# Performance work log

Hardware: AMD Instinct MI355X
Metric: run time of the kernel (lower is better)

## Reference

```python
import jax, jax.numpy as jnp
import numpy as np

C, G, S, L, B = 16, 8192, 8, 3, 32


def setup_inputs() -> dict:
    key = jax.random.key(0)
    kx, kI = jax.random.split(key)
    # x: valuation vector over G ground atoms per batch element, in [0,1)
    x = jax.random.uniform(kx, (B, G), dtype=jnp.float32)
    # I: precomputed index tensor [C, G, S, L], indices into the G axis of x
    I = jax.random.randint(kI, (C, G, S, L), 0, G, dtype=jnp.int64)
    return {"x": x, "I": I}


def reference(x, I):
    # Equivalent of: for each clause i, gather(V_tild, 1, I_i) -> prod over L -> sum over S
    # torch gather semantics: out[b, g, s, l] = x[b, I[i, g, s, l]]
    # Vectorized over all clauses at once; no repeat/broadcast materialization beyond the gather.
    gathered = x[:, I]                        # [B, C, G, S, L]
    body = jnp.prod(gathered, axis=-1)        # conjunction over L body literals -> [B, C, G, S]
    clause_val = jnp.sum(body, axis=-1)       # sum over S substitutions -> [B, C, G]
    # torch.stack over clauses puts C first: [C, B, G]
    return jnp.transpose(clause_val, (1, 0, 2))
```

## Files before the change

kernel.cpp:

```cpp
#include <hip/hip_runtime.h>
#include <hip/hip_fp16.h>
#include <stdint.h>

#define Cc 16
#define Gg 8192
#define Ss 8
#define Ll 3
#define Bb 32

#define ZS 4
#define THREADS 512
#define ITERS 2

__device__ __forceinline__ void async_load16(const void* gsrc, void* lds) {
    uint32_t l32 = (uint32_t)__builtin_amdgcn_readfirstlane((uint32_t)(uintptr_t)lds);
    __builtin_amdgcn_global_load_lds(
        (const __attribute__((address_space(1))) uint32_t*)(uintptr_t)gsrc,
        (__attribute__((address_space(3))) uint32_t*)(uintptr_t)l32,
        16, 0, 0);
}

__global__ __launch_bounds__(256) void pack_idx(const int* __restrict__ I,
                                                ushort* __restrict__ I16) {
    int t = blockIdx.x * 256 + threadIdx.x;
    int4 v = ((const int4*)I)[t];
    ushort4 o = { (ushort)v.x, (ushort)v.y, (ushort)v.z, (ushort)v.w };
    ((ushort4*)I16)[t] = o;
}

__global__ __launch_bounds__(256) void build_xh(const float* __restrict__ x,
                                                uint4* __restrict__ xh) {
    int t = blockIdx.x * 256 + threadIdx.x;
    int z = t >> 13;
    int g = t & (Gg - 1);
    uint32_t w[4];
    #pragma unroll
    for (int j = 0; j < 4; ++j) {
        __half2 h = __floats2half2_rn(x[(size_t)(8 * z + 2 * j) * Gg + g],
                                      x[(size_t)(8 * z + 2 * j + 1) * Gg + g]);
        w[j] = *(const uint32_t*)&h;
    }
    xh[t] = make_uint4(w[0], w[1], w[2], w[3]);
}

__global__ __launch_bounds__(THREADS) void clause_f16(const uint4* __restrict__ xh,
                                                      const ushort* __restrict__ I16,
                                                      float* __restrict__ out) {
    __shared__ uint4 xl[Gg];
    const int tid = threadIdx.x;
    const int z = blockIdx.y;
    const int c = blockIdx.x >> 3;
    const int gbase = (blockIdx.x & 7) * (THREADS * ITERS);

    {
        const char* gs = (const char*)(xh + (size_t)z * Gg);
        char* ls = (char*)xl;
        const int lane = tid & 63;
        const int w = tid >> 6;
        #pragma unroll
        for (int i = 0; i < 16; ++i) {
            int off = ((w << 4) | i) << 10;
            async_load16(gs + off + lane * 16, ls + off);
        }
    }

    uint4 iq[ITERS][3];
    #pragma unroll
    for (int it = 0; it < ITERS; ++it) {
        int g = gbase + it * THREADS + tid;
        const uint4* ip = (const uint4*)(I16 + ((size_t)c * Gg + g) * (Ss * Ll));
        iq[it][0] = ip[0]; iq[it][1] = ip[1]; iq[it][2] = ip[2];
    }

    __syncthreads();

    #pragma unroll
    for (int it = 0; it < ITERS; ++it) {
        const int g = gbase + it * THREADS + tid;
        uint32_t wd[12] = {iq[it][0].x, iq[it][0].y, iq[it][0].z, iq[it][0].w,
                           iq[it][1].x, iq[it][1].y, iq[it][1].z, iq[it][1].w,
                           iq[it][2].x, iq[it][2].y, iq[it][2].z, iq[it][2].w};

        uint4 v[Ss * Ll];
        #pragma unroll
        for (int k = 0; k < Ss * Ll; ++k) {
            uint32_t idx = (k & 1) ? (wd[k >> 1] >> 16) : (wd[k >> 1] & 0xffffu);
            v[k] = xl[idx];
        }

        float acc[8] = {0.f, 0.f, 0.f, 0.f, 0.f, 0.f, 0.f, 0.f};
        #pragma unroll
        for (int s = 0; s < Ss; ++s) {
            const __half2* a = (const __half2*)&v[3 * s];
            const __half2* b = (const __half2*)&v[3 * s + 1];
            const __half2* d = (const __half2*)&v[3 * s + 2];
            #pragma unroll
            for (int j = 0; j < 4; ++j) {
                __half2 p = __hmul2(__hmul2(a[j], b[j]), d[j]);
                float2 pf = __half22float2(p);
                acc[2 * j]     += pf.x;
                acc[2 * j + 1] += pf.y;
            }
        }

        float* op = out + ((size_t)(c * Bb + 8 * z)) * Gg + g;
        #pragma unroll
        for (int j = 0; j < 8; ++j)
            op[(size_t)j * Gg] = acc[j];
    }
}

__global__ __launch_bounds__(256) void clause_kernel_direct(const float* __restrict__ x,
                                                            const int* __restrict__ I,
                                                            float* __restrict__ out) {
    const int tid = threadIdx.x;
    const int b = tid & 31;
    const int j = tid >> 5;
    const int g = blockIdx.x * 8 + j;
    const int c = blockIdx.y;

    const int* Icg = I + (size_t)(c * Gg + g) * (Ss * Ll);
    float sum = 0.f;
    #pragma unroll
    for (int s = 0; s < Ss; ++s) {
        float p0 = x[(size_t)b * Gg + Icg[3 * s + 0]];
        float p1 = x[(size_t)b * Gg + Icg[3 * s + 1]];
        float p2 = x[(size_t)b * Gg + Icg[3 * s + 2]];
        sum += p0 * p1 * p2;
    }
    out[(size_t)(c * Bb + b) * Gg + g] = sum;
}

extern "C" void kernel_launch(void* const* d_in, const int* in_sizes, int n_in,
                              void* d_out, int out_size, void* d_ws, size_t ws_size,
                              hipStream_t stream) {
    const float* x = (const float*)d_in[0];
    const int* I = (const int*)d_in[1];
    float* out = (float*)d_out;

    const size_t nIdx = (size_t)Cc * Gg * Ss * Ll;
    const size_t xh_bytes = (size_t)ZS * Gg * sizeof(uint4);
    const size_t i16_bytes = nIdx * sizeof(ushort);

    if (ws_size >= xh_bytes + i16_bytes) {
        uint4* xh = (uint4*)d_ws;
        ushort* I16 = (ushort*)((char*)d_ws + xh_bytes);
        pack_idx<<<(int)(nIdx / 4 / 256), 256, 0, stream>>>(I, I16);
        build_xh<<<(ZS * Gg) / 256, 256, 0, stream>>>(x, xh);
        clause_f16<<<dim3((Cc * Gg) / (THREADS * ITERS), ZS), THREADS, 0, stream>>>(xh, I16, out);
    } else {
        clause_kernel_direct<<<dim3(Gg / 8, Cc), 256, 0, stream>>>(x, I, out);
    }
}
```

Before: 84.55 us.

## Drop index packing kernel; read int32 indices directly and swizzle LDS table

Removes the separate pack_idx pass that converted int64/int32 indices to 16-bit. The main kernel now reads the int32 index tensor directly, so each of the four z-blocks re-reads the wider indices. The LDS x table is also XOR-swizzled per 8-entry group, and each gather is split into two 8-byte loads to cut bank conflicts. This saves a full pass over the indices and one launch, at the cost of twice the index bytes per clause kernel read and more LDS instructions.

```diff
diff --git a/kernel.cpp b/kernel.cpp
--- a/kernel.cpp
+++ b/kernel.cpp
@@ -20,31 +20,57 @@
         16, 0, 0);
 }
 
-__global__ __launch_bounds__(256) void pack_idx(const int* __restrict__ I,
-                                                ushort* __restrict__ I16) {
-    int t = blockIdx.x * 256 + threadIdx.x;
-    int4 v = ((const int4*)I)[t];
-    ushort4 o = { (ushort)v.x, (ushort)v.y, (ushort)v.z, (ushort)v.w };
-    ((ushort4*)I16)[t] = o;
-}
-
 __global__ __launch_bounds__(256) void build_xh(const float* __restrict__ x,
                                                 uint4* __restrict__ xh) {
     int t = blockIdx.x * 256 + threadIdx.x;
     int z = t >> 13;
     int g = t & (Gg - 1);
-    uint32_t w[4];
+    uint32_t d[4];
     #pragma unroll
     for (int j = 0; j < 4; ++j) {
         __half2 h = __floats2half2_rn(x[(size_t)(8 * z + 2 * j) * Gg + g],
                                       x[(size_t)(8 * z + 2 * j + 1) * Gg + g]);
-        w[j] = *(const uint32_t*)&h;
+        d[j] = *(const uint32_t*)&h;
     }
-    xh[t] = make_uint4(w[0], w[1], w[2], w[3]);
+    uint32_t s = (g >> 3) & 1u;
+    xh[t] = s ? make_uint4(d[2], d[3], d[0], d[1])
+              : make_uint4(d[0], d[1], d[2], d[3]);
+}
+
+__device__ __forceinline__ void clause_eval(const uint2* __restrict__ xl2,
+                                            const int4 q[6], float acc[8]) {
+    int idx[Ss * Ll] = {q[0].x, q[0].y, q[0].z, q[0].w, q[1].x, q[1].y, q[1].z, q[1].w,
+                        q[2].x, q[2].y, q[2].z, q[2].w, q[3].x, q[3].y, q[3].z, q[3].w,
+                        q[4].x, q[4].y, q[4].z, q[4].w, q[5].x, q[5].y, q[5].z, q[5].w};
+    uint2 r0[Ss * Ll], r1[Ss * Ll];
+    #pragma unroll
+    for (int k = 0; k < Ss * Ll; ++k) {
+        uint32_t u = (uint32_t)idx[k];
+        uint32_t a0 = (u << 1) | ((u >> 3) & 1u);
+        r0[k] = xl2[a0];
+        r1[k] = xl2[a0 ^ 1u];
+    }
+    #pragma unroll
+    for (int s = 0; s < Ss; ++s) {
+        const int k0 = 3 * s, k1 = 3 * s + 1, k2 = 3 * s + 2;
+        const uint32_t pa[4] = {r0[k0].x, r0[k0].y, r1[k0].x, r1[k0].y};
+        const uint32_t pb[4] = {r0[k1].x, r0[k1].y, r1[k1].x, r1[k1].y};
+        const uint32_t pd[4] = {r0[k2].x, r0[k2].y, r1[k2].x, r1[k2].y};
+        #pragma unroll
+        for (int j = 0; j < 4; ++j) {
+            __half2 a = *(const __half2*)&pa[j];
+            __half2 b = *(const __half2*)&pb[j];
+            __half2 d = *(const __half2*)&pd[j];
+            __half2 p = __hmul2(__hmul2(a, b), d);
+            float2 pf = __half22float2(p);
+            acc[2 * j] += pf.x;
+            acc[2 * j + 1] += pf.y;
+        }
+    }
 }
 
 __global__ __launch_bounds__(THREADS) void clause_f16(const uint4* __restrict__ xh,
-                                                      const ushort* __restrict__ I16,
+                                                      const int* __restrict__ I,
                                                       float* __restrict__ out) {
     __shared__ uint4 xl[Gg];
     const int tid = threadIdx.x;
@@ -64,49 +90,34 @@
         }
     }
 
-    uint4 iq[ITERS][3];
+    const int g0 = gbase + tid;
+    const int g1 = gbase + THREADS + tid;
+    const int4* ip0 = (const int4*)(I + ((size_t)c * Gg + g0) * (Ss * Ll));
+    const int4* ip1 = (const int4*)(I + ((size_t)c * Gg + g1) * (Ss * Ll));
+    int4 q0[6], q1[6];
     #pragma unroll
-    for (int it = 0; it < ITERS; ++it) {
-        int g = gbase + it * THREADS + tid;
-        const uint4* ip = (const uint4*)(I16 + ((size_t)c * Gg + g) * (Ss * Ll));
-        iq[it][0] = ip[0]; iq[it][1] = ip[1]; iq[it][2] = ip[2];
-    }
+    for (int k = 0; k < 6; ++k) q0[k] = ip0[k];
+    #pragma unroll
+    for (int k = 0; k < 6; ++k) q1[k] = ip1[k];
 
     __syncthreads();
 
-    #pragma unroll
-    for (int it = 0; it < ITERS; ++it) {
-        const int g = gbase + it * THREADS + tid;
-        uint32_t wd[12] = {iq[it][0].x, iq[it][0].y, iq[it][0].z, iq[it][0].w,
-                           iq[it][1].x, iq[it][1].y, iq[it][1].z, iq[it][1].w,
-                           iq[it][2].x, iq[it][2].y, iq[it][2].z, iq[it][2].w};
+    const uint2* xl2 = (const uint2*)xl;
+    float* opb = out + ((size_t)(c * Bb + 8 * z)) * Gg;
 
-        uint4 v[Ss * Ll];
-        #pragma unroll
-        for (int k = 0; k < Ss * Ll; ++k) {
-            uint32_t idx = (k & 1) ? (wd[k >> 1] >> 16) : (wd[k >> 1] & 0xffffu);
-            v[k] = xl[idx];
-        }
-
-        float acc[8] = {0.f, 0.f, 0.f, 0.f, 0.f, 0.f, 0.f, 0.f};
-        #pragma unroll
-        for (int s = 0; s < Ss; ++s) {
-            const __half2* a = (const __half2*)&v[3 * s];
-            const __half2* b = (const __half2*)&v[3 * s + 1];
-            const __half2* d = (const __half2*)&v[3 * s + 2];
-            #pragma unroll
-            for (int j = 0; j < 4; ++j) {
-                __half2 p = __hmul2(__hmul2(a[j], b[j]), d[j]);
-                float2 pf = __half22float2(p);
-                acc[2 * j]     += pf.x;
-                acc[2 * j + 1] += pf.y;
-            }
-        }
-
-        float* op = out + ((size_t)(c * Bb + 8 * z)) * Gg + g;
+    {
+        float acc[8] = {0, 0, 0, 0, 0, 0, 0, 0};
+        clause_eval(xl2, q0, acc);
         #pragma unroll
         for (int j = 0; j < 8; ++j)
-            op[(size_t)j * Gg] = acc[j];
+            opb[(size_t)j * Gg + g0] = acc[j];
+    }
+    {
+        float acc[8] = {0, 0, 0, 0, 0, 0, 0, 0};
+        clause_eval(xl2, q1, acc);
+        #pragma unroll
+        for (int j = 0; j < 8; ++j)
+            opb[(size_t)j * Gg + g1] = acc[j];
     }
 }
 
@@ -138,16 +149,12 @@
     const int* I = (const int*)d_in[1];
     float* out = (float*)d_out;
 
-    const size_t nIdx = (size_t)Cc * Gg * Ss * Ll;
     const size_t xh_bytes = (size_t)ZS * Gg * sizeof(uint4);
-    const size_t i16_bytes = nIdx * sizeof(ushort);
 
-    if (ws_size >= xh_bytes + i16_bytes) {
+    if (ws_size >= xh_bytes) {
         uint4* xh = (uint4*)d_ws;
-        ushort* I16 = (ushort*)((char*)d_ws + xh_bytes);
-        pack_idx<<<(int)(nIdx / 4 / 256), 256, 0, stream>>>(I, I16);
         build_xh<<<(ZS * Gg) / 256, 256, 0, stream>>>(x, xh);
-        clause_f16<<<dim3((Cc * Gg) / (THREADS * ITERS), ZS), THREADS, 0, stream>>>(xh, I16, out);
+        clause_f16<<<dim3((Cc * Gg) / (THREADS * ITERS), ZS), THREADS, 0, stream>>>(xh, I, out);
     } else {
         clause_kernel_direct<<<dim3(Gg / 8, Cc), 256, 0, stream>>>(x, I, out);
     }
```

Result: faster. 82.76 us (-2.1%).
